# Performance work log

Hardware: AMD Instinct MI355X
Metric: run time of the kernel (lower is better)

The kernel has to match this reference:

```python
import jax, jax.numpy as jnp
import numpy as np

EPS = 1e-5

def _gn(x, w, b):
    # GroupNorm with 1 group on [N, C]: normalize each row over C, then affine.
    mu = jnp.mean(x, axis=-1, keepdims=True)
    var = jnp.mean((x - mu) ** 2, axis=-1, keepdims=True)
    return (x - mu) * jax.lax.rsqrt(var + EPS) * w + b

def setup_inputs() -> dict:
    key = jax.random.key(0)
    ks = jax.random.split(key, 24)
    N_AGT, N_CTX, E, D, NC = 50000, 100000, 500000, 128, 2
    s = 0.05  # weight init scale
    inp = {
        "agts": jax.random.normal(ks[0], (N_AGT, D), jnp.float32),
        "ctx": jax.random.normal(ks[1], (N_CTX, D), jnp.float32),
        "agt_ctrs": jax.random.normal(ks[2], (N_AGT, NC), jnp.float32),
        "ctx_ctrs": jax.random.normal(ks[3], (N_CTX, NC), jnp.float32),
        "hi": jax.random.randint(ks[4], (E,), 0, N_AGT, jnp.int32),
        "wi": jax.random.randint(ks[5], (E,), 0, N_CTX, jnp.int32),
        # dist MLP: Linear(2->128, bias) + ReLU, then Linear(128->128 no bias)+GN+ReLU
        "Wd1": jax.random.normal(ks[6], (D, NC), jnp.float32) * s,
        "bd1": jnp.zeros((D,), jnp.float32),
        "Wd2": jax.random.normal(ks[7], (D, D), jnp.float32) * s,
        "gd2w": jnp.ones((D,), jnp.float32), "gd2b": jnp.zeros((D,), jnp.float32),
        # query: Linear(128->128 no bias)+GN+ReLU
        "Wq": jax.random.normal(ks[8], (D, D), jnp.float32) * s,
        "gqw": jnp.ones((D,), jnp.float32), "gqb": jnp.zeros((D,), jnp.float32),
        # ctx MLP: Linear(384->128 no bias)+GN+ReLU, then Linear(128->128 no bias)
        "Wc1": jax.random.normal(ks[9], (D, 3 * D), jnp.float32) * s,
        "gc1w": jnp.ones((D,), jnp.float32), "gc1b": jnp.zeros((D,), jnp.float32),
        "Wc2": jax.random.normal(ks[10], (D, D), jnp.float32) * s,
        # agt linear (no bias), post-scatter GN, final Linear(no bias)+GN
        "Wa": jax.random.normal(ks[11], (D, D), jnp.float32) * s,
        "gnw": jnp.ones((D,), jnp.float32), "gnb": jnp.zeros((D,), jnp.float32),
        "Wl": jax.random.normal(ks[12], (D, D), jnp.float32) * s,
        "glw": jnp.ones((D,), jnp.float32), "glb": jnp.zeros((D,), jnp.float32),
    }
    return inp

def reference(agts, ctx, agt_ctrs, ctx_ctrs, hi, wi,
              Wd1, bd1, Wd2, gd2w, gd2b, Wq, gqw, gqb,
              Wc1, gc1w, gc1b, Wc2, Wa, gnw, gnb, Wl, glw, glb):
    res = agts
    # dist branch: relative center offsets of edges -> MLP
    d = agt_ctrs[hi] - ctx_ctrs[wi]                    # [E, 2]
    d = jax.nn.relu(d @ Wd1.T + bd1)                   # [E, 128]
    d = jax.nn.relu(_gn(d @ Wd2.T, gd2w, gd2b))        # [E, 128]
    # query branch: gathered agent features
    q = jax.nn.relu(_gn(agts[hi] @ Wq.T, gqw, gqb))    # [E, 128]
    # ctx branch: concat(dist, query, gathered ctx) -> MLP
    c = jnp.concatenate([d, q, ctx[wi]], axis=1)       # [E, 384]
    c = jax.nn.relu(_gn(c @ Wc1.T, gc1w, gc1b))        # [E, 128]
    c = c @ Wc2.T                                      # [E, 128]
    # scatter-add messages back to agents
    a = agts @ Wa.T
    a = a.at[hi].add(c)
    a = jax.nn.relu(_gn(a, gnw, gnb))
    a = _gn(a @ Wl.T, glw, glb)
    return jax.nn.relu(a + res)
```

## Files before the change

kernel.cpp:

```cpp
#include <hip/hip_runtime.h>
#include <hip/hip_bf16.h>

#define D 128
#define TM 64
#define APITCH 136
#define SPITCH 129

typedef __attribute__((ext_vector_type(8))) short short8;
typedef __attribute__((ext_vector_type(4))) float f32x4;

__device__ __forceinline__ short f2bf(float f) {
    union { float f; unsigned u; } v; v.f = f;
    unsigned r = v.u + 0x7fffu + ((v.u >> 16) & 1u);
    return (short)(r >> 16);
}

struct TileLDS {
    short A[TM * APITCH];
    float S[TM * SPITCH];
    float red1[TM][4];
    float red2[TM][4];
    float mean_s[TM];
    float rstd_s[TM];
    int hi_s[TM];
    int wi_s[TM];
};

__device__ __forceinline__ short8 load_bfrag(const float* p) {
    short8 r;
#pragma unroll
    for (int j = 0; j < 8; ++j) r[j] = f2bf(p[j]);
    return r;
}

__device__ __forceinline__ void load_wset(const float* W, int pitch, int n0, int lr, int kh,
                                          short8 frag[2][4]) {
#pragma unroll
    for (int t = 0; t < 2; ++t)
#pragma unroll
        for (int ks = 0; ks < 4; ++ks)
            frag[t][ks] = load_bfrag(W + (size_t)(n0 + t * 16 + lr) * pitch + ks * 32 + kh * 8);
}

__device__ __forceinline__ void wave_gemm(const short* A, const short8 frag[2][4],
                                          int lr, int kh, f32x4 acc[4][2]) {
#pragma unroll
    for (int mt = 0; mt < 4; ++mt)
#pragma unroll
        for (int t = 0; t < 2; ++t)
            acc[mt][t] = (f32x4){0.f, 0.f, 0.f, 0.f};
#pragma unroll
    for (int ks = 0; ks < 4; ++ks) {
        short8 a[4];
#pragma unroll
        for (int mt = 0; mt < 4; ++mt)
            a[mt] = *(const short8*)&A[(mt * 16 + lr) * APITCH + ks * 32 + kh * 8];
#pragma unroll
        for (int mt = 0; mt < 4; ++mt)
#pragma unroll
            for (int t = 0; t < 2; ++t)
                acc[mt][t] = __builtin_amdgcn_mfma_f32_16x16x32_bf16(a[mt], frag[t][ks], acc[mt][t], 0, 0, 0);
    }
}

__device__ __forceinline__ void stage_acc(float* S, const f32x4 acc[4][2], int lane, int w) {
    int lr = lane & 15, hh = lane >> 4;
#pragma unroll
    for (int mt = 0; mt < 4; ++mt)
#pragma unroll
        for (int t = 0; t < 2; ++t)
#pragma unroll
            for (int r = 0; r < 4; ++r)
                S[(mt * 16 + hh * 4 + r) * SPITCH + w * 32 + t * 16 + lr] = acc[mt][t][r];
}

__device__ __forceinline__ void store_acc_global(float* Y, long rbase, int M,
                                                 const f32x4 acc[4][2], int lane, int w) {
    int lr = lane & 15, hh = lane >> 4;
#pragma unroll
    for (int mt = 0; mt < 4; ++mt)
#pragma unroll
        for (int t = 0; t < 2; ++t)
#pragma unroll
            for (int r = 0; r < 4; ++r) {
                int row = mt * 16 + hh * 4 + r;
                if (rbase + row < M)
                    Y[(size_t)(rbase + row) * D + w * 32 + t * 16 + lr] = acc[mt][t][r];
            }
}

__device__ __forceinline__ void gn_to_A(TileLDS& L, const float* gw, const float* gb, int tid) {
    int row = tid >> 2, q = tid & 3;
    float* Srow = &L.S[row * SPITCH];
    float s = 0.f, ss = 0.f;
#pragma unroll
    for (int c = q * 32; c < q * 32 + 32; ++c) { float v = Srow[c]; s += v; ss += v * v; }
    L.red1[row][q] = s; L.red2[row][q] = ss;
    __syncthreads();
    if (tid < TM) {
        float sum = L.red1[tid][0] + L.red1[tid][1] + L.red1[tid][2] + L.red1[tid][3];
        float sq  = L.red2[tid][0] + L.red2[tid][1] + L.red2[tid][2] + L.red2[tid][3];
        float mu = sum * (1.f / 128.f);
        float var = sq * (1.f / 128.f) - mu * mu;
        L.mean_s[tid] = mu;
        L.rstd_s[tid] = rsqrtf(var + 1e-5f);
    }
    __syncthreads();
    float mu = L.mean_s[row], rs = L.rstd_s[row];
#pragma unroll
    for (int c = q * 32; c < q * 32 + 32; ++c) {
        float v = (Srow[c] - mu) * rs * gw[c] + gb[c];
        L.A[row * APITCH + c] = f2bf(fmaxf(v, 0.f));
    }
    __syncthreads();
}

__device__ __forceinline__ void gn_gather_to_A(TileLDS& L, const float* gw, const float* gb,
                                               const float* qpart, const float* cpart, int tid) {
    int row = tid >> 2, q = tid & 3;
    float* Srow = &L.S[row * SPITCH];
    const float* qp = qpart + (size_t)L.hi_s[row] * D;
    const float* cp = cpart + (size_t)L.wi_s[row] * D;
    float s = 0.f, ss = 0.f;
#pragma unroll
    for (int c = q * 32; c < q * 32 + 32; ++c) {
        float v = Srow[c] + qp[c] + cp[c];
        Srow[c] = v; s += v; ss += v * v;
    }
    L.red1[row][q] = s; L.red2[row][q] = ss;
    __syncthreads();
    if (tid < TM) {
        float sum = L.red1[tid][0] + L.red1[tid][1] + L.red1[tid][2] + L.red1[tid][3];
        float sq  = L.red2[tid][0] + L.red2[tid][1] + L.red2[tid][2] + L.red2[tid][3];
        float mu = sum * (1.f / 128.f);
        float var = sq * (1.f / 128.f) - mu * mu;
        L.mean_s[tid] = mu;
        L.rstd_s[tid] = rsqrtf(var + 1e-5f);
    }
    __syncthreads();
    float mu = L.mean_s[row], rs = L.rstd_s[row];
#pragma unroll
    for (int c = q * 32; c < q * 32 + 32; ++c) {
        float v = (Srow[c] - mu) * rs * gw[c] + gb[c];
        L.A[row * APITCH + c] = f2bf(fmaxf(v, 0.f));
    }
    __syncthreads();
}

__device__ __forceinline__ void stage_rows_to_A(TileLDS& L, const float* X, long rbase, int M, int tid) {
#pragma unroll
    for (int it = 0; it < 8; ++it) {
        int chunk = tid + it * 256;
        int row = chunk >> 5, c4 = chunk & 31;
        long r = rbase + row;
        float4 v = (r < M) ? *(const float4*)&X[(size_t)r * D + c4 * 4] : make_float4(0.f, 0.f, 0.f, 0.f);
        short* a = &L.A[row * APITCH + c4 * 4];
        a[0] = f2bf(v.x); a[1] = f2bf(v.y); a[2] = f2bf(v.z); a[3] = f2bf(v.w);
    }
}

__device__ __forceinline__ void stage_rows_to_S(TileLDS& L, const float* X, long rbase, int M, int tid) {
#pragma unroll
    for (int it = 0; it < 8; ++it) {
        int chunk = tid + it * 256;
        int row = chunk >> 5, c4 = chunk & 31;
        long r = rbase + row;
        float4 v = (r < M) ? *(const float4*)&X[(size_t)r * D + c4 * 4] : make_float4(0.f, 0.f, 0.f, 0.f);
        float* s = &L.S[row * SPITCH + c4 * 4];
        s[0] = v.x; s[1] = v.y; s[2] = v.z; s[3] = v.w;
    }
}

__global__ __launch_bounds__(256, 2)
void k_qpath(const float* __restrict__ agts,
             const float* __restrict__ Wq, const float* __restrict__ gqw, const float* __restrict__ gqb,
             const float* __restrict__ Wc1, const float* __restrict__ Wa,
             float* __restrict__ qpart, float* __restrict__ abuf, int M, int ntiles) {
    __shared__ TileLDS L;
    int tid = threadIdx.x;
    int lane = tid & 63, w = tid >> 6;
    int lr = lane & 15, kh = lane >> 4;
    int n0 = w * 32;
    short8 fa[2][4], fq[2][4], fcq[2][4];
    load_wset(Wa, 128, n0, lr, kh, fa);
    load_wset(Wq, 128, n0, lr, kh, fq);
    load_wset(Wc1 + 128, 384, n0, lr, kh, fcq);

    for (int tile = blockIdx.x; tile < ntiles; tile += gridDim.x) {
        long rbase = (long)tile * TM;
        stage_rows_to_A(L, agts, rbase, M, tid);
        __syncthreads();
        f32x4 acc[4][2];
        wave_gemm(L.A, fa, lr, kh, acc);
        store_acc_global(abuf, rbase, M, acc, lane, w);
        wave_gemm(L.A, fq, lr, kh, acc);
        stage_acc(L.S, acc, lane, w);
        __syncthreads();
        gn_to_A(L, gqw, gqb, tid);
        wave_gemm(L.A, fcq, lr, kh, acc);
        store_acc_global(qpart, rbase, M, acc, lane, w);
        __syncthreads();
    }
}

__global__ __launch_bounds__(256, 2)
void k_ctx(const float* __restrict__ ctx, const float* __restrict__ Wc1,
           float* __restrict__ cpart, int M, int ntiles) {
    __shared__ TileLDS L;
    int tid = threadIdx.x;
    int lane = tid & 63, w = tid >> 6;
    int lr = lane & 15, kh = lane >> 4;
    short8 fc[2][4];
    load_wset(Wc1 + 256, 384, w * 32, lr, kh, fc);
    for (int tile = blockIdx.x; tile < ntiles; tile += gridDim.x) {
        long rbase = (long)tile * TM;
        stage_rows_to_A(L, ctx, rbase, M, tid);
        __syncthreads();
        f32x4 acc[4][2];
        wave_gemm(L.A, fc, lr, kh, acc);
        store_acc_global(cpart, rbase, M, acc, lane, w);
        __syncthreads();
    }
}

__global__ __launch_bounds__(256, 2)
void k_edge(const float* __restrict__ agt_ctrs, const float* __restrict__ ctx_ctrs,
            const int* __restrict__ hi, const int* __restrict__ wi,
            const float* __restrict__ Wd1, const float* __restrict__ bd1,
            const float* __restrict__ Wd2, const float* __restrict__ gd2w, const float* __restrict__ gd2b,
            const float* __restrict__ Wc1, const float* __restrict__ gc1w, const float* __restrict__ gc1b,
            const float* __restrict__ Wc2,
            const float* __restrict__ qpart, const float* __restrict__ cpart,
            float* __restrict__ abuf, int E, int ntiles) {
    __shared__ TileLDS L;
    int tid = threadIdx.x;
    int lane = tid & 63, w = tid >> 6;
    int lr = lane & 15, kh = lane >> 4;
    int n0 = w * 32;
    short8 fd2[2][4], fc1[2][4], fc2[2][4];
    load_wset(Wd2, 128, n0, lr, kh, fd2);
    load_wset(Wc1, 384, n0, lr, kh, fc1);
    load_wset(Wc2, 128, n0, lr, kh, fc2);

    for (int tile = blockIdx.x; tile < ntiles; tile += gridDim.x) {
        long ebase = (long)tile * TM;
        if (tid < TM) {
            long e = ebase + tid;
            L.hi_s[tid] = (e < E) ? hi[e] : 0;
            L.wi_s[tid] = (e < E) ? wi[e] : 0;
        }
        __syncthreads();
        {
            int row = tid >> 2, q = tid & 3;
            long e = ebase + row;
            float dd0 = 0.f, dd1 = 0.f;
            int h = L.hi_s[row], c = L.wi_s[row];
            if (e < E) {
                dd0 = agt_ctrs[h * 2 + 0] - ctx_ctrs[c * 2 + 0];
                dd1 = agt_ctrs[h * 2 + 1] - ctx_ctrs[c * 2 + 1];
            }
#pragma unroll
            for (int cc = q * 32; cc < q * 32 + 32; ++cc) {
                float v = (e < E) ? fmaxf(Wd1[cc * 2 + 0] * dd0 + Wd1[cc * 2 + 1] * dd1 + bd1[cc], 0.f) : 0.f;
                L.A[row * APITCH + cc] = f2bf(v);
            }
        }
        __syncthreads();
        f32x4 acc[4][2];
        wave_gemm(L.A, fd2, lr, kh, acc);
        stage_acc(L.S, acc, lane, w);
        __syncthreads();
        gn_to_A(L, gd2w, gd2b, tid);
        wave_gemm(L.A, fc1, lr, kh, acc);
        stage_acc(L.S, acc, lane, w);
        __syncthreads();
        gn_gather_to_A(L, gc1w, gc1b, qpart, cpart, tid);
        wave_gemm(L.A, fc2, lr, kh, acc);
#pragma unroll
        for (int mt = 0; mt < 4; ++mt)
#pragma unroll
            for (int r = 0; r < 4; ++r) {
                int erow = mt * 16 + kh * 4 + r;
                long e = ebase + erow;
                if (e < E) {
                    size_t base = (size_t)L.hi_s[erow] * D;
#pragma unroll
                    for (int t = 0; t < 2; ++t)
                        atomicAdd(&abuf[base + n0 + t * 16 + lr], acc[mt][t][r]);
                }
            }
        __syncthreads();
    }
}

__global__ __launch_bounds__(256, 2)
void k_final(const float* __restrict__ abuf, const float* __restrict__ agts,
             const float* __restrict__ Wl,
             const float* __restrict__ gnw, const float* __restrict__ gnb,
             const float* __restrict__ glw, const float* __restrict__ glb,
             float* __restrict__ out, int M, int ntiles) {
    __shared__ TileLDS L;
    int tid = threadIdx.x;
    int lane = tid & 63, w = tid >> 6;
    int lr = lane & 15, kh = lane >> 4;
    short8 fl[2][4];
    load_wset(Wl, 128, w * 32, lr, kh, fl);
    for (int tile = blockIdx.x; tile < ntiles; tile += gridDim.x) {
        long rbase = (long)tile * TM;
        stage_rows_to_S(L, abuf, rbase, M, tid);
        __syncthreads();
        gn_to_A(L, gnw, gnb, tid);
        f32x4 acc[4][2];
        wave_gemm(L.A, fl, lr, kh, acc);
        stage_acc(L.S, acc, lane, w);
        __syncthreads();
        {
            int row = tid >> 2, q = tid & 3;
            float* Srow = &L.S[row * SPITCH];
            float s = 0.f, ss = 0.f;
#pragma unroll
            for (int c = q * 32; c < q * 32 + 32; ++c) { float v = Srow[c]; s += v; ss += v * v; }
            L.red1[row][q] = s; L.red2[row][q] = ss;
            __syncthreads();
            if (tid < TM) {
                float sum = L.red1[tid][0] + L.red1[tid][1] + L.red1[tid][2] + L.red1[tid][3];
                float sq  = L.red2[tid][0] + L.red2[tid][1] + L.red2[tid][2] + L.red2[tid][3];
                float mu = sum * (1.f / 128.f);
                float var = sq * (1.f / 128.f) - mu * mu;
                L.mean_s[tid] = mu;
                L.rstd_s[tid] = rsqrtf(var + 1e-5f);
            }
            __syncthreads();
            long r = rbase + row;
            if (r < M) {
                float mu = L.mean_s[row], rs = L.rstd_s[row];
                const float* res = &agts[(size_t)r * D];
                float* o = &out[(size_t)r * D];
#pragma unroll
                for (int c = q * 32; c < q * 32 + 32; ++c) {
                    float v = (Srow[c] - mu) * rs * glw[c] + glb[c];
                    o[c] = fmaxf(v + res[c], 0.f);
                }
            }
            __syncthreads();
        }
    }
}

extern "C" void kernel_launch(void* const* d_in, const int* in_sizes, int n_in,
                              void* d_out, int out_size, void* d_ws, size_t ws_size,
                              hipStream_t stream) {
    const float* agts     = (const float*)d_in[0];
    const float* ctx      = (const float*)d_in[1];
    const float* agt_ctrs = (const float*)d_in[2];
    const float* ctx_ctrs = (const float*)d_in[3];
    const int*   hi       = (const int*)d_in[4];
    const int*   wi       = (const int*)d_in[5];
    const float* Wd1 = (const float*)d_in[6];
    const float* bd1 = (const float*)d_in[7];
    const float* Wd2 = (const float*)d_in[8];
    const float* gd2w = (const float*)d_in[9];
    const float* gd2b = (const float*)d_in[10];
    const float* Wq  = (const float*)d_in[11];
    const float* gqw = (const float*)d_in[12];
    const float* gqb = (const float*)d_in[13];
    const float* Wc1 = (const float*)d_in[14];
    const float* gc1w = (const float*)d_in[15];
    const float* gc1b = (const float*)d_in[16];
    const float* Wc2 = (const float*)d_in[17];
    const float* Wa  = (const float*)d_in[18];
    const float* gnw = (const float*)d_in[19];
    const float* gnb = (const float*)d_in[20];
    const float* Wl  = (const float*)d_in[21];
    const float* glw = (const float*)d_in[22];
    const float* glb = (const float*)d_in[23];

    int N_AGT = in_sizes[0] / D;
    int N_CTX = in_sizes[1] / D;
    int E     = in_sizes[4];
    float* out = (float*)d_out;

    float* qpart = (float*)d_ws;
    float* cpart = qpart + (size_t)N_AGT * D;
    float* abuf  = cpart + (size_t)N_CTX * D;

    int tq = (N_AGT + TM - 1) / TM;
    int tc = (N_CTX + TM - 1) / TM;
    int te = (E + TM - 1) / TM;

    k_qpath<<<tq, 256, 0, stream>>>(agts, Wq, gqw, gqb, Wc1, Wa, qpart, abuf, N_AGT, tq);
    k_ctx<<<tc, 256, 0, stream>>>(ctx, Wc1, cpart, N_CTX, tc);
    k_edge<<<te, 256, 0, stream>>>(agt_ctrs, ctx_ctrs, hi, wi, Wd1, bd1,
                                   Wd2, gd2w, gd2b, Wc1, gc1w, gc1b, Wc2,
                                   qpart, cpart, abuf, E, te);
    k_final<<<tq, 256, 0, stream>>>(abuf, agts, Wl, gnw, gnb, glw, glb, out, N_AGT, tq);
}
```

Measured before the change: 968.2 us.

## Compute GroupNorm directly from MFMA accumulators, dropping the LDS staging buffer

The fp32 S staging tile in LDS is removed. GroupNorm statistics are now computed straight from the MFMA accumulator registers using lane shuffles plus a small cross-wave reduction, and the normalized bf16 result is written directly into the A tile. The edge kernel adds the gathered qpart/cpart rows to the accumulators in registers, and the final kernel keeps abuf rows in registers and writes its output from the accumulators. The smaller LDS footprint lets the launch bounds rise to 3–4 blocks per CU, aiming to cut LDS traffic and barriers and raise occupancy, at the risk of register pressure and less-coalesced per-lane gathers.

```diff
diff --git a/kernel.cpp b/kernel.cpp
--- a/kernel.cpp
+++ b/kernel.cpp
@@ -4,10 +4,10 @@
 #define D 128
 #define TM 64
 #define APITCH 136
-#define SPITCH 129
 
 typedef __attribute__((ext_vector_type(8))) short short8;
 typedef __attribute__((ext_vector_type(4))) float f32x4;
+typedef __attribute__((ext_vector_type(2))) float f32x2;
 
 __device__ __forceinline__ short f2bf(float f) {
     union { float f; unsigned u; } v; v.f = f;
@@ -17,11 +17,8 @@
 
 struct TileLDS {
     short A[TM * APITCH];
-    float S[TM * SPITCH];
-    float red1[TM][4];
-    float red2[TM][4];
-    float mean_s[TM];
-    float rstd_s[TM];
+    f32x2 red[TM][4][4];
+    f32x2 mr[TM];
     int hi_s[TM];
     int wi_s[TM];
 };
@@ -61,17 +58,6 @@
             for (int t = 0; t < 2; ++t)
                 acc[mt][t] = __builtin_amdgcn_mfma_f32_16x16x32_bf16(a[mt], frag[t][ks], acc[mt][t], 0, 0, 0);
     }
-}
-
-__device__ __forceinline__ void stage_acc(float* S, const f32x4 acc[4][2], int lane, int w) {
-    int lr = lane & 15, hh = lane >> 4;
-#pragma unroll
-    for (int mt = 0; mt < 4; ++mt)
-#pragma unroll
-        for (int t = 0; t < 2; ++t)
-#pragma unroll
-            for (int r = 0; r < 4; ++r)
-                S[(mt * 16 + hh * 4 + r) * SPITCH + w * 32 + t * 16 + lr] = acc[mt][t][r];
 }
 
 __device__ __forceinline__ void store_acc_global(float* Y, long rbase, int M,
@@ -89,61 +75,51 @@
             }
 }
 
-__device__ __forceinline__ void gn_to_A(TileLDS& L, const float* gw, const float* gb, int tid) {
-    int row = tid >> 2, q = tid & 3;
-    float* Srow = &L.S[row * SPITCH];
-    float s = 0.f, ss = 0.f;
-#pragma unroll
-    for (int c = q * 32; c < q * 32 + 32; ++c) { float v = Srow[c]; s += v; ss += v * v; }
-    L.red1[row][q] = s; L.red2[row][q] = ss;
+__device__ __forceinline__ void gn_stats(TileLDS& L, const f32x4 acc[4][2],
+                                         int tid, int lane, int w) {
+    int lr = lane & 15, hh = lane >> 4;
+#pragma unroll
+    for (int mt = 0; mt < 4; ++mt)
+#pragma unroll
+        for (int r = 0; r < 4; ++r) {
+            float s = acc[mt][0][r] + acc[mt][1][r];
+            float q = acc[mt][0][r] * acc[mt][0][r] + acc[mt][1][r] * acc[mt][1][r];
+            s += __shfl_xor(s, 1); q += __shfl_xor(q, 1);
+            s += __shfl_xor(s, 2); q += __shfl_xor(q, 2);
+            if ((lr & 3) == mt) {
+                int row = mt * 16 + hh * 4 + r;
+                L.red[row][w][lr >> 2] = (f32x2){s, q};
+            }
+        }
     __syncthreads();
     if (tid < TM) {
-        float sum = L.red1[tid][0] + L.red1[tid][1] + L.red1[tid][2] + L.red1[tid][3];
-        float sq  = L.red2[tid][0] + L.red2[tid][1] + L.red2[tid][2] + L.red2[tid][3];
-        float mu = sum * (1.f / 128.f);
-        float var = sq * (1.f / 128.f) - mu * mu;
-        L.mean_s[tid] = mu;
-        L.rstd_s[tid] = rsqrtf(var + 1e-5f);
+        float s = 0.f, q = 0.f;
+        const f32x2* p = (const f32x2*)L.red[tid];
+#pragma unroll
+        for (int i = 0; i < 16; ++i) { f32x2 v = p[i]; s += v[0]; q += v[1]; }
+        float mu = s * (1.f / 128.f);
+        float var = q * (1.f / 128.f) - mu * mu;
+        L.mr[tid] = (f32x2){mu, rsqrtf(var + 1e-5f)};
     }
     __syncthreads();
-    float mu = L.mean_s[row], rs = L.rstd_s[row];
-#pragma unroll
-    for (int c = q * 32; c < q * 32 + 32; ++c) {
-        float v = (Srow[c] - mu) * rs * gw[c] + gb[c];
-        L.A[row * APITCH + c] = f2bf(fmaxf(v, 0.f));
-    }
-    __syncthreads();
-}
-
-__device__ __forceinline__ void gn_gather_to_A(TileLDS& L, const float* gw, const float* gb,
-                                               const float* qpart, const float* cpart, int tid) {
-    int row = tid >> 2, q = tid & 3;
-    float* Srow = &L.S[row * SPITCH];
-    const float* qp = qpart + (size_t)L.hi_s[row] * D;
-    const float* cp = cpart + (size_t)L.wi_s[row] * D;
-    float s = 0.f, ss = 0.f;
-#pragma unroll
-    for (int c = q * 32; c < q * 32 + 32; ++c) {
-        float v = Srow[c] + qp[c] + cp[c];
-        Srow[c] = v; s += v; ss += v * v;
-    }
-    L.red1[row][q] = s; L.red2[row][q] = ss;
-    __syncthreads();
-    if (tid < TM) {
-        float sum = L.red1[tid][0] + L.red1[tid][1] + L.red1[tid][2] + L.red1[tid][3];
-        float sq  = L.red2[tid][0] + L.red2[tid][1] + L.red2[tid][2] + L.red2[tid][3];
-        float mu = sum * (1.f / 128.f);
-        float var = sq * (1.f / 128.f) - mu * mu;
-        L.mean_s[tid] = mu;
-        L.rstd_s[tid] = rsqrtf(var + 1e-5f);
-    }
-    __syncthreads();
-    float mu = L.mean_s[row], rs = L.rstd_s[row];
-#pragma unroll
-    for (int c = q * 32; c < q * 32 + 32; ++c) {
-        float v = (Srow[c] - mu) * rs * gw[c] + gb[c];
-        L.A[row * APITCH + c] = f2bf(fmaxf(v, 0.f));
-    }
+}
+
+__device__ __forceinline__ void gn_reg(TileLDS& L, const f32x4 acc[4][2],
+                                       float gw0, float gb0, float gw1, float gb1,
+                                       int tid, int lane, int w) {
+    gn_stats(L, acc, tid, lane, w);
+    int lr = lane & 15, hh = lane >> 4, n0 = w * 32;
+#pragma unroll
+    for (int mt = 0; mt < 4; ++mt)
+#pragma unroll
+        for (int r = 0; r < 4; ++r) {
+            int row = mt * 16 + hh * 4 + r;
+            f32x2 m = L.mr[row];
+            float v0 = (acc[mt][0][r] - m[0]) * m[1] * gw0 + gb0;
+            float v1 = (acc[mt][1][r] - m[0]) * m[1] * gw1 + gb1;
+            L.A[row * APITCH + n0 + lr]      = f2bf(fmaxf(v0, 0.f));
+            L.A[row * APITCH + n0 + 16 + lr] = f2bf(fmaxf(v1, 0.f));
+        }
     __syncthreads();
 }
 
@@ -159,19 +135,7 @@
     }
 }
 
-__device__ __forceinline__ void stage_rows_to_S(TileLDS& L, const float* X, long rbase, int M, int tid) {
-#pragma unroll
-    for (int it = 0; it < 8; ++it) {
-        int chunk = tid + it * 256;
-        int row = chunk >> 5, c4 = chunk & 31;
-        long r = rbase + row;
-        float4 v = (r < M) ? *(const float4*)&X[(size_t)r * D + c4 * 4] : make_float4(0.f, 0.f, 0.f, 0.f);
-        float* s = &L.S[row * SPITCH + c4 * 4];
-        s[0] = v.x; s[1] = v.y; s[2] = v.z; s[3] = v.w;
-    }
-}
-
-__global__ __launch_bounds__(256, 2)
+__global__ __launch_bounds__(256, 3)
 void k_qpath(const float* __restrict__ agts,
              const float* __restrict__ Wq, const float* __restrict__ gqw, const float* __restrict__ gqb,
              const float* __restrict__ Wc1, const float* __restrict__ Wa,
@@ -185,6 +149,8 @@
     load_wset(Wa, 128, n0, lr, kh, fa);
     load_wset(Wq, 128, n0, lr, kh, fq);
     load_wset(Wc1 + 128, 384, n0, lr, kh, fcq);
+    float gw0 = gqw[n0 + lr], gw1 = gqw[n0 + 16 + lr];
+    float gb0 = gqb[n0 + lr], gb1 = gqb[n0 + 16 + lr];
 
     for (int tile = blockIdx.x; tile < ntiles; tile += gridDim.x) {
         long rbase = (long)tile * TM;
@@ -194,16 +160,14 @@
         wave_gemm(L.A, fa, lr, kh, acc);
         store_acc_global(abuf, rbase, M, acc, lane, w);
         wave_gemm(L.A, fq, lr, kh, acc);
-        stage_acc(L.S, acc, lane, w);
-        __syncthreads();
-        gn_to_A(L, gqw, gqb, tid);
+        gn_reg(L, acc, gw0, gb0, gw1, gb1, tid, lane, w);
         wave_gemm(L.A, fcq, lr, kh, acc);
         store_acc_global(qpart, rbase, M, acc, lane, w);
         __syncthreads();
     }
 }
 
-__global__ __launch_bounds__(256, 2)
+__global__ __launch_bounds__(256, 4)
 void k_ctx(const float* __restrict__ ctx, const float* __restrict__ Wc1,
            float* __restrict__ cpart, int M, int ntiles) {
     __shared__ TileLDS L;
@@ -223,7 +187,7 @@
     }
 }
 
-__global__ __launch_bounds__(256, 2)
+__global__ __launch_bounds__(256, 3)
 void k_edge(const float* __restrict__ agt_ctrs, const float* __restrict__ ctx_ctrs,
             const int* __restrict__ hi, const int* __restrict__ wi,
             const float* __restrict__ Wd1, const float* __restrict__ bd1,
@@ -241,6 +205,10 @@
     load_wset(Wd2, 128, n0, lr, kh, fd2);
     load_wset(Wc1, 384, n0, lr, kh, fc1);
     load_wset(Wc2, 128, n0, lr, kh, fc2);
+    float g2w0 = gd2w[n0 + lr], g2w1 = gd2w[n0 + 16 + lr];
+    float g2b0 = gd2b[n0 + lr], g2b1 = gd2b[n0 + 16 + lr];
+    float g1w0 = gc1w[n0 + lr], g1w1 = gc1w[n0 + 16 + lr];
+    float g1b0 = gc1b[n0 + lr], g1b1 = gc1b[n0 + 16 + lr];
 
     for (int tile = blockIdx.x; tile < ntiles; tile += gridDim.x) {
         long ebase = (long)tile * TM;
@@ -249,32 +217,44 @@
             L.hi_s[tid] = (e < E) ? hi[e] : 0;
             L.wi_s[tid] = (e < E) ? wi[e] : 0;
         }
-        __syncthreads();
         {
-            int row = tid >> 2, q = tid & 3;
+            int row = tid >> 2, q4 = tid & 3;
             long e = ebase + row;
+            bool valid = e < E;
             float dd0 = 0.f, dd1 = 0.f;
-            int h = L.hi_s[row], c = L.wi_s[row];
-            if (e < E) {
+            if (valid) {
+                int h = hi[e], c = wi[e];
                 dd0 = agt_ctrs[h * 2 + 0] - ctx_ctrs[c * 2 + 0];
                 dd1 = agt_ctrs[h * 2 + 1] - ctx_ctrs[c * 2 + 1];
             }
 #pragma unroll
-            for (int cc = q * 32; cc < q * 32 + 32; ++cc) {
-                float v = (e < E) ? fmaxf(Wd1[cc * 2 + 0] * dd0 + Wd1[cc * 2 + 1] * dd1 + bd1[cc], 0.f) : 0.f;
-                L.A[row * APITCH + cc] = f2bf(v);
+            for (int cb = 0; cb < 4; ++cb) {
+                short8 ov;
+#pragma unroll
+                for (int j = 0; j < 8; ++j) {
+                    int c = q4 * 32 + cb * 8 + j;
+                    float v = valid ? fmaxf(Wd1[c * 2 + 0] * dd0 + Wd1[c * 2 + 1] * dd1 + bd1[c], 0.f) : 0.f;
+                    ov[j] = f2bf(v);
+                }
+                *(short8*)&L.A[row * APITCH + q4 * 32 + cb * 8] = ov;
             }
         }
         __syncthreads();
         f32x4 acc[4][2];
         wave_gemm(L.A, fd2, lr, kh, acc);
-        stage_acc(L.S, acc, lane, w);
-        __syncthreads();
-        gn_to_A(L, gd2w, gd2b, tid);
+        gn_reg(L, acc, g2w0, g2b0, g2w1, g2b1, tid, lane, w);
         wave_gemm(L.A, fc1, lr, kh, acc);
-        stage_acc(L.S, acc, lane, w);
-        __syncthreads();
-        gn_gather_to_A(L, gc1w, gc1b, qpart, cpart, tid);
+#pragma unroll
+        for (int mt = 0; mt < 4; ++mt)
+#pragma unroll
+            for (int r = 0; r < 4; ++r) {
+                int row = mt * 16 + kh * 4 + r;
+                const float* qp = qpart + (size_t)L.hi_s[row] * D;
+                const float* cp = cpart + (size_t)L.wi_s[row] * D;
+                acc[mt][0][r] += qp[n0 + lr]      + cp[n0 + lr];
+                acc[mt][1][r] += qp[n0 + 16 + lr] + cp[n0 + 16 + lr];
+            }
+        gn_reg(L, acc, g1w0, g1b0, g1w1, g1b1, tid, lane, w);
         wave_gemm(L.A, fc2, lr, kh, acc);
 #pragma unroll
         for (int mt = 0; mt < 4; ++mt)
@@ -284,16 +264,15 @@
                 long e = ebase + erow;
                 if (e < E) {
                     size_t base = (size_t)L.hi_s[erow] * D;
-#pragma unroll
-                    for (int t = 0; t < 2; ++t)
-                        atomicAdd(&abuf[base + n0 + t * 16 + lr], acc[mt][t][r]);
+                    atomicAdd(&abuf[base + n0 + lr],      acc[mt][0][r]);
+                    atomicAdd(&abuf[base + n0 + 16 + lr], acc[mt][1][r]);
                 }
             }
         __syncthreads();
     }
 }
 
-__global__ __launch_bounds__(256, 2)
+__global__ __launch_bounds__(256, 4)
 void k_final(const float* __restrict__ abuf, const float* __restrict__ agts,
              const float* __restrict__ Wl,
              const float* __restrict__ gnw, const float* __restrict__ gnb,
@@ -303,47 +282,74 @@
     int tid = threadIdx.x;
     int lane = tid & 63, w = tid >> 6;
     int lr = lane & 15, kh = lane >> 4;
+    int n0 = w * 32;
     short8 fl[2][4];
-    load_wset(Wl, 128, w * 32, lr, kh, fl);
+    load_wset(Wl, 128, n0, lr, kh, fl);
+    float gw0 = glw[n0 + lr], gw1 = glw[n0 + 16 + lr];
+    float gb0 = glb[n0 + lr], gb1 = glb[n0 + 16 + lr];
+
     for (int tile = blockIdx.x; tile < ntiles; tile += gridDim.x) {
         long rbase = (long)tile * TM;
-        stage_rows_to_S(L, abuf, rbase, M, tid);
-        __syncthreads();
-        gn_to_A(L, gnw, gnb, tid);
+        int row = tid >> 2, q4 = tid & 3;
+        long r = rbase + row;
+        float x[32];
+        {
+            float s = 0.f, q = 0.f;
+            const float4* src = (const float4*)(abuf + (size_t)r * D + q4 * 32);
+#pragma unroll
+            for (int i = 0; i < 8; ++i) {
+                float4 v = (r < M) ? src[i] : make_float4(0.f, 0.f, 0.f, 0.f);
+                x[i * 4 + 0] = v.x; x[i * 4 + 1] = v.y; x[i * 4 + 2] = v.z; x[i * 4 + 3] = v.w;
+                s += v.x + v.y + v.z + v.w;
+                q += v.x * v.x + v.y * v.y + v.z * v.z + v.w * v.w;
+            }
+            L.red[row][q4][0] = (f32x2){s, q};
+        }
+        __syncthreads();
+        if (tid < TM) {
+            float s = 0.f, q = 0.f;
+#pragma unroll
+            for (int i = 0; i < 4; ++i) { f32x2 v = L.red[tid][i][0]; s += v[0]; q += v[1]; }
+            float mu = s * (1.f / 128.f);
+            float var = q * (1.f / 128.f) - mu * mu;
+            L.mr[tid] = (f32x2){mu, rsqrtf(var + 1e-5f)};
+        }
+        __syncthreads();
+        {
+            f32x2 m = L.mr[row];
+#pragma unroll
+            for (int cb = 0; cb < 4; ++cb) {
+                short8 ov;
+#pragma unroll
+                for (int j = 0; j < 8; ++j) {
+                    int c = q4 * 32 + cb * 8 + j;
+                    float v = (x[cb * 8 + j] - m[0]) * m[1] * gnw[c] + gnb[c];
+                    ov[j] = f2bf(fmaxf(v, 0.f));
+                }
+                *(short8*)&L.A[row * APITCH + q4 * 32 + cb * 8] = ov;
+            }
+        }
+        __syncthreads();
         f32x4 acc[4][2];
         wave_gemm(L.A, fl, lr, kh, acc);
-        stage_acc(L.S, acc, lane, w);
-        __syncthreads();
-        {
-            int row = tid >> 2, q = tid & 3;
-            float* Srow = &L.S[row * SPITCH];
-            float s = 0.f, ss = 0.f;
-#pragma unroll
-            for (int c = q * 32; c < q * 32 + 32; ++c) { float v = Srow[c]; s += v; ss += v * v; }
-            L.red1[row][q] = s; L.red2[row][q] = ss;
-            __syncthreads();
-            if (tid < TM) {
-                float sum = L.red1[tid][0] + L.red1[tid][1] + L.red1[tid][2] + L.red1[tid][3];
-                float sq  = L.red2[tid][0] + L.red2[tid][1] + L.red2[tid][2] + L.red2[tid][3];
-                float mu = sum * (1.f / 128.f);
-                float var = sq * (1.f / 128.f) - mu * mu;
-                L.mean_s[tid] = mu;
-                L.rstd_s[tid] = rsqrtf(var + 1e-5f);
-            }
-            __syncthreads();
-            long r = rbase + row;
-            if (r < M) {
-                float mu = L.mean_s[row], rs = L.rstd_s[row];
-                const float* res = &agts[(size_t)r * D];
-                float* o = &out[(size_t)r * D];
-#pragma unroll
-                for (int c = q * 32; c < q * 32 + 32; ++c) {
-                    float v = (Srow[c] - mu) * rs * glw[c] + glb[c];
-                    o[c] = fmaxf(v + res[c], 0.f);
+        gn_stats(L, acc, tid, lane, w);
+#pragma unroll
+        for (int mt = 0; mt < 4; ++mt)
+#pragma unroll
+            for (int rr = 0; rr < 4; ++rr) {
+                int orow = mt * 16 + kh * 4 + rr;
+                long gr = rbase + orow;
+                if (gr < M) {
+                    f32x2 m = L.mr[orow];
+                    float v0 = (acc[mt][0][rr] - m[0]) * m[1] * gw0 + gb0;
+                    float v1 = (acc[mt][1][rr] - m[0]) * m[1] * gw1 + gb1;
+                    v0 += agts[(size_t)gr * D + n0 + lr];
+                    v1 += agts[(size_t)gr * D + n0 + 16 + lr];
+                    out[(size_t)gr * D + n0 + lr]      = fmaxf(v0, 0.f);
+                    out[(size_t)gr * D + n0 + 16 + lr] = fmaxf(v1, 0.f);
                 }
             }
-            __syncthreads();
-        }
+        __syncthreads();
     }
 }
 
```

Measured after the change: 1.023 ms. 5.7% more time.
